# Kernel optimization log

Measured on AMD Instinct MI355X. Metric: run time of the kernel, lower is better.

Reference implementation:

```python
import jax, jax.numpy as jnp
import numpy as np

ALPHA = 0.5
DIM = -1
TOL = 1e-4
MAX_ITER = 5000


def stable_log_w(y, alpha):
    """Halley's method root of h(x) = -alpha*x + (y-alpha) - (1-alpha)*exp(x)."""

    def resid(x):
        return -alpha * x + (y - alpha) - (1.0 - alpha) * jnp.exp(x)

    x0 = jnp.minimum(y / alpha - 1.0, y - 1.0)

    def cond(st):
        x, it = st
        # torch breaks when max|f| <= tol -> continue while > tol
        return (jnp.max(jnp.abs(resid(x))) > TOL) & (it < MAX_ITER)

    def body(st):
        x, it = st
        e = jnp.exp(x)
        f = -alpha * x + (y - alpha) - (1.0 - alpha) * e
        df = -alpha - (1.0 - alpha) * e
        ddf = -(1.0 - alpha) * e
        x = x - 2.0 * f * df / (2.0 * df * df - f * ddf)
        return (x, it + 1)

    x, _ = jax.lax.while_loop(cond, body, (x0, jnp.int32(0)))
    return x


def prox_softmax_core(y, alpha, dim):
    """Newton over nu s.t. sum_i exp(g(y_i + nu)) = 1. Returns (p, nu, l)."""

    def eval_at(nu):
        l = stable_log_w(y + nu, alpha)
        p = jnp.exp(l)
        f = jnp.sum(p, axis=dim, keepdims=True) - 1.0
        return l, p, f

    nu0 = 1.0 - jnp.max(y, axis=dim, keepdims=True)
    l0, p0, f0 = eval_at(nu0)

    def cond(st):
        nu, l, p, f, it = st
        # torch breaks when max|f| < tol -> continue while >= tol
        return (jnp.max(jnp.abs(f)) >= TOL) & (it < MAX_ITER)

    def body(st):
        nu, l, p, f, it = st
        df = jnp.sum(p / (y + nu - alpha * l), axis=dim, keepdims=True)
        nu = nu - f / df
        l, p, f = eval_at(nu)
        return (nu, l, p, f, it + 1)

    nu, l, p, f, _ = jax.lax.while_loop(cond, body, (nu0, l0, p0, f0, jnp.int32(0)))
    return p, nu, l


def setup_inputs() -> dict:
    key = jax.random.key(0)
    x = jax.random.normal(key, (8192, 4096), dtype=jnp.float32)
    return {"x": x}


def reference(x):
    p, _, _ = prox_softmax_core(x, ALPHA, DIM)
    return p
```

## Files before the change

### kernel.cpp

```cpp
#include <hip/hip_runtime.h>
#include <math.h>

#define TPB 256
#define NWAVE 4
#define EPT 16
#define COLS 4096
#define RPB 4

typedef float vfloat4 __attribute__((ext_vector_type(4)));

__device__ __forceinline__ float wave_sum(float v) {
#pragma unroll
    for (int o = 32; o > 0; o >>= 1) v += __shfl_xor(v, o, 64);
    return v;
}
__device__ __forceinline__ float wave_max(float v) {
#pragma unroll
    for (int o = 32; o > 0; o >>= 1) v = fmaxf(v, __shfl_xor(v, o, 64));
    return v;
}

__device__ __forceinline__ void block_red2_h(float& a, float& b, volatile float* sred, int wid, int lane) {
    a = wave_sum(a); b = wave_sum(b);
    if (lane == 0) { sred[20 + wid] = a; sred[24 + wid] = b; }
    __syncthreads();
    a = (sred[20] + sred[21]) + (sred[22] + sred[23]);
    b = (sred[24] + sred[25]) + (sred[26] + sred[27]);
    __syncthreads();
}

__device__ __forceinline__ float halley_hw(float p, float t) {
    float e = __expf(p);
    float w = p * e;
    float f = w - t;
    float fp = w + e;
    float den = fmaf(fp, fp, -0.5f * f * (fp + e));
    return p - __fdividef(f * fp, den);
}

__global__ __launch_bounds__(TPB) void prox_softmax_kernel(
    const float* __restrict__ X, float* __restrict__ P, int rows)
{
    __shared__ float sred[28];
    const int tid = threadIdx.x;
    const int wid = tid >> 6, lane = tid & 63;
    const int row0 = blockIdx.x * RPB;
    const float C2E = 2.8853900817779268f;

    float cur[EPT], nxt[EPT];

    {
        const float4* __restrict__ x4 = reinterpret_cast<const float4*>(X + (size_t)row0 * COLS);
#pragma unroll
        for (int j = 0; j < 4; ++j) {
            float4 v = x4[tid + j * TPB];
            cur[4 * j + 0] = v.x; cur[4 * j + 1] = v.y;
            cur[4 * j + 2] = v.z; cur[4 * j + 3] = v.w;
        }
    }

    for (int r = 0; r < RPB; ++r) {
        const int row = row0 + r;
        if (row >= rows) return;
        const float4* __restrict__ x4 = reinterpret_cast<const float4*>(X + (size_t)row * COLS);
        vfloat4* __restrict__ p4 = reinterpret_cast<vfloat4*>(P + (size_t)row * COLS);

        if (r + 1 < RPB && row + 1 < rows) {
            const float4* __restrict__ x4n = reinterpret_cast<const float4*>(X + (size_t)(row + 1) * COLS);
#pragma unroll
            for (int j = 0; j < 4; ++j) {
                float4 v = x4n[tid + j * TPB];
                nxt[4 * j + 0] = v.x; nxt[4 * j + 1] = v.y;
                nxt[4 * j + 2] = v.z; nxt[4 * j + 3] = v.w;
            }
        }

        float A = 0.f, B = 0.f, qm = 0.f;
#pragma unroll
        for (int j = 0; j < EPT; ++j) {
            float e = __builtin_amdgcn_exp2f(cur[j] * C2E);
            cur[j] = e;
            A += e;
            B = fmaf(e, e, B);
            qm = fmaxf(qm, e);
        }

        A = wave_sum(A); B = wave_sum(B); qm = wave_max(qm);
        if (lane == 0) { sred[wid] = A; sred[4 + wid] = B; sred[8 + wid] = qm; }
        __syncthreads();
        A  = (sred[0] + sred[1]) + (sred[2] + sred[3]);
        B  = (sred[4] + sred[5]) + (sred[6] + sred[7]);
        qm = fmaxf(fmaxf(sred[8], sred[9]), fmaxf(sred[10], sred[11]));

        float disc = fmaf(A, A, -4.f * B);
        float s = __fdividef(2.f, A + sqrtf(fmaxf(disc, 0.f)));

        float S1 = 0.f, S2 = 0.f;
#pragma unroll
        for (int j = 0; j < EPT; ++j) {
            float t = cur[j] * s;
            float acc = fmaf(23.343054f, t, -10.8f);
            acc = fmaf(acc, t, 125.f / 24.f);
            acc = fmaf(acc, t, -8.f / 3.f);
            acc = fmaf(acc, t, 1.5f);
            acc = fmaf(acc, t, -1.f);
            acc = fmaf(acc, t, 1.f);
            float pp = t * acc;
            cur[j] = pp;
            S1 += pp;
            S2 += pp * fmaf(pp, pp - 1.f, 1.f);
        }

        S1 = wave_sum(S1); S2 = wave_sum(S2);
        if (lane == 0) { sred[12 + wid] = S1; sred[16 + wid] = S2; }
        __syncthreads();
        S1 = (sred[12] + sred[13]) + (sred[14] + sred[15]);
        S2 = (sred[16] + sred[17]) + (sred[18] + sred[19]);

        float f = S1 - 1.f;
        float tmax = qm * s;

        if ((tmax < 0.22f) && (fabsf(f) < 0.05f)) {
            float dsig = -__fdividef(f, S2);
#pragma unroll
            for (int j = 0; j < EPT; ++j) {
                float pp = cur[j];
                float rr = pp * fmaf(pp, pp - 1.f, 1.f);
                cur[j] = fmaf(rr, dsig, pp);
            }
        } else {
            float ls = __log2f(s);
#pragma unroll
            for (int j = 0; j < 4; ++j) {
                float4 v = x4[tid + j * TPB];
#pragma unroll
                for (int k = 0; k < 4; ++k) {
                    float xv = (k == 0) ? v.x : (k == 1) ? v.y : (k == 2) ? v.z : v.w;
                    float t = __builtin_amdgcn_exp2f(fmaf(xv, C2E, ls));
                    cur[4 * j + k] = __logf(1.f + t);
                }
            }
            for (int it = 0; it < 10; ++it) {
                S1 = 0.f; S2 = 0.f;
                float ls2 = __log2f(s);
#pragma unroll
                for (int j = 0; j < 4; ++j) {
                    float4 v = x4[tid + j * TPB];
#pragma unroll
                    for (int k = 0; k < 4; ++k) {
                        float xv = (k == 0) ? v.x : (k == 1) ? v.y : (k == 2) ? v.z : v.w;
                        float t = __builtin_amdgcn_exp2f(fmaf(xv, C2E, ls2));
                        float pp = halley_hw(cur[4 * j + k], t);
                        pp = halley_hw(pp, t);
                        cur[4 * j + k] = pp;
                        S1 += pp;
                        S2 += __fdividef(pp, 1.f + pp);
                    }
                }
                block_red2_h(S1, S2, sred, wid, lane);
                f = S1 - 1.f;
                if (fabsf(f) < 2e-5f) break;
                float dsig = fminf(fmaxf(-__fdividef(f, S2), -1.f), 1.f);
                s *= __expf(dsig);
            }
        }

#pragma unroll
        for (int j = 0; j < 4; ++j) {
            vfloat4 v;
            v.x = cur[4 * j + 0]; v.y = cur[4 * j + 1];
            v.z = cur[4 * j + 2]; v.w = cur[4 * j + 3];
            __builtin_nontemporal_store(v, &p4[tid + j * TPB]);
        }

        if (r + 1 < RPB) {
#pragma unroll
            for (int j = 0; j < EPT; ++j) cur[j] = nxt[j];
        }
    }
}

extern "C" void kernel_launch(void* const* d_in, const int* in_sizes, int n_in,
                              void* d_out, int out_size, void* d_ws, size_t ws_size,
                              hipStream_t stream) {
    const float* x = (const float*)d_in[0];
    float* out = (float*)d_out;
    int rows = out_size / COLS;
    int blocks = (rows + RPB - 1) / RPB;
    prox_softmax_kernel<<<blocks, TPB, 0, stream>>>(x, out, rows);
}
```

Before: 56.47 us.

## Process two rows per block interleaved, merging their reductions into shared barriers

Switches from four rows per block processed sequentially with next-row prefetch to two rows per block processed together. Both rows' exp, series and reduction steps are interleaved so their block reductions share a single barrier, which halves the number of barriers per row and exposes more independent work to each thread. The grid doubles to rows/2 blocks. In exchange, register pressure rises from holding two 16-element rows, there is no longer an odd-row tail guard, and the __syncthreads inside divergent heavy-path branches depends on the branch condition being uniform across the block.

```diff
diff --git a/kernel.cpp b/kernel.cpp
--- a/kernel.cpp
+++ b/kernel.cpp
@@ -2,10 +2,8 @@
 #include <math.h>
 
 #define TPB 256
-#define NWAVE 4
 #define EPT 16
 #define COLS 4096
-#define RPB 4
 
 typedef float vfloat4 __attribute__((ext_vector_type(4)));
 
@@ -18,15 +16,6 @@
 #pragma unroll
     for (int o = 32; o > 0; o >>= 1) v = fmaxf(v, __shfl_xor(v, o, 64));
     return v;
-}
-
-__device__ __forceinline__ void block_red2_h(float& a, float& b, volatile float* sred, int wid, int lane) {
-    a = wave_sum(a); b = wave_sum(b);
-    if (lane == 0) { sred[20 + wid] = a; sred[24 + wid] = b; }
-    __syncthreads();
-    a = (sred[20] + sred[21]) + (sred[22] + sred[23]);
-    b = (sred[24] + sred[25]) + (sred[26] + sred[27]);
-    __syncthreads();
 }
 
 __device__ __forceinline__ float halley_hw(float p, float t) {
@@ -38,145 +27,171 @@
     return p - __fdividef(f * fp, den);
 }
 
+__device__ __forceinline__ float w_series(float t) {
+    float acc = fmaf(23.343054f, t, -10.8f);
+    acc = fmaf(acc, t, 125.f / 24.f);
+    acc = fmaf(acc, t, -8.f / 3.f);
+    acc = fmaf(acc, t, 1.5f);
+    acc = fmaf(acc, t, -1.f);
+    acc = fmaf(acc, t, 1.f);
+    return t * acc;
+}
+
+__device__ __forceinline__ void heavy_solve(
+    const float4* __restrict__ x4, float* qq, float& s,
+    volatile float* sred, int tid, int wid, int lane, float C2E)
+{
+    float ls = __log2f(s);
+#pragma unroll
+    for (int j = 0; j < 4; ++j) {
+        float4 v = x4[tid + j * TPB];
+#pragma unroll
+        for (int k = 0; k < 4; ++k) {
+            float xv = (k == 0) ? v.x : (k == 1) ? v.y : (k == 2) ? v.z : v.w;
+            float t = __builtin_amdgcn_exp2f(fmaf(xv, C2E, ls));
+            qq[4 * j + k] = __logf(1.f + t);
+        }
+    }
+    for (int it = 0; it < 10; ++it) {
+        float S1 = 0.f, S2 = 0.f;
+        float ls2 = __log2f(s);
+#pragma unroll
+        for (int j = 0; j < 4; ++j) {
+            float4 v = x4[tid + j * TPB];
+#pragma unroll
+            for (int k = 0; k < 4; ++k) {
+                float xv = (k == 0) ? v.x : (k == 1) ? v.y : (k == 2) ? v.z : v.w;
+                float t = __builtin_amdgcn_exp2f(fmaf(xv, C2E, ls2));
+                float pp = halley_hw(qq[4 * j + k], t);
+                pp = halley_hw(pp, t);
+                qq[4 * j + k] = pp;
+                S1 += pp;
+                S2 += __fdividef(pp, 1.f + pp);
+            }
+        }
+        S1 = wave_sum(S1); S2 = wave_sum(S2);
+        if (lane == 0) { sred[40 + wid] = S1; sred[44 + wid] = S2; }
+        __syncthreads();
+        S1 = (sred[40] + sred[41]) + (sred[42] + sred[43]);
+        S2 = (sred[44] + sred[45]) + (sred[46] + sred[47]);
+        __syncthreads();
+        float f = S1 - 1.f;
+        if (fabsf(f) < 2e-5f) break;
+        float dsig = fminf(fmaxf(-__fdividef(f, S2), -1.f), 1.f);
+        s *= __expf(dsig);
+    }
+}
+
 __global__ __launch_bounds__(TPB) void prox_softmax_kernel(
     const float* __restrict__ X, float* __restrict__ P, int rows)
 {
-    __shared__ float sred[28];
+    __shared__ float sred[48];
     const int tid = threadIdx.x;
     const int wid = tid >> 6, lane = tid & 63;
-    const int row0 = blockIdx.x * RPB;
+    const int row0 = blockIdx.x * 2;
+    const int row1 = row0 + 1;
     const float C2E = 2.8853900817779268f;
 
-    float cur[EPT], nxt[EPT];
-
-    {
-        const float4* __restrict__ x4 = reinterpret_cast<const float4*>(X + (size_t)row0 * COLS);
-#pragma unroll
-        for (int j = 0; j < 4; ++j) {
-            float4 v = x4[tid + j * TPB];
-            cur[4 * j + 0] = v.x; cur[4 * j + 1] = v.y;
-            cur[4 * j + 2] = v.z; cur[4 * j + 3] = v.w;
-        }
-    }
-
-    for (int r = 0; r < RPB; ++r) {
-        const int row = row0 + r;
-        if (row >= rows) return;
-        const float4* __restrict__ x4 = reinterpret_cast<const float4*>(X + (size_t)row * COLS);
-        vfloat4* __restrict__ p4 = reinterpret_cast<vfloat4*>(P + (size_t)row * COLS);
-
-        if (r + 1 < RPB && row + 1 < rows) {
-            const float4* __restrict__ x4n = reinterpret_cast<const float4*>(X + (size_t)(row + 1) * COLS);
-#pragma unroll
-            for (int j = 0; j < 4; ++j) {
-                float4 v = x4n[tid + j * TPB];
-                nxt[4 * j + 0] = v.x; nxt[4 * j + 1] = v.y;
-                nxt[4 * j + 2] = v.z; nxt[4 * j + 3] = v.w;
-            }
-        }
-
-        float A = 0.f, B = 0.f, qm = 0.f;
+    const float4* __restrict__ xa = reinterpret_cast<const float4*>(X + (size_t)row0 * COLS);
+    const float4* __restrict__ xb = reinterpret_cast<const float4*>(X + (size_t)row1 * COLS);
+    vfloat4* __restrict__ pa = reinterpret_cast<vfloat4*>(P + (size_t)row0 * COLS);
+    vfloat4* __restrict__ pb = reinterpret_cast<vfloat4*>(P + (size_t)row1 * COLS);
+
+    float a[EPT], b[EPT];
+
+#pragma unroll
+    for (int j = 0; j < 4; ++j) {
+        float4 va = xa[tid + j * TPB];
+        float4 vb = xb[tid + j * TPB];
+        a[4 * j + 0] = va.x; a[4 * j + 1] = va.y; a[4 * j + 2] = va.z; a[4 * j + 3] = va.w;
+        b[4 * j + 0] = vb.x; b[4 * j + 1] = vb.y; b[4 * j + 2] = vb.z; b[4 * j + 3] = vb.w;
+    }
+
+    float A0 = 0.f, B0 = 0.f, m0 = 0.f;
+    float A1 = 0.f, B1 = 0.f, m1 = 0.f;
+#pragma unroll
+    for (int j = 0; j < EPT; ++j) {
+        float e0 = __builtin_amdgcn_exp2f(a[j] * C2E);
+        float e1 = __builtin_amdgcn_exp2f(b[j] * C2E);
+        a[j] = e0; b[j] = e1;
+        A0 += e0;             A1 += e1;
+        B0 = fmaf(e0, e0, B0); B1 = fmaf(e1, e1, B1);
+        m0 = fmaxf(m0, e0);   m1 = fmaxf(m1, e1);
+    }
+
+    A0 = wave_sum(A0); A1 = wave_sum(A1);
+    B0 = wave_sum(B0); B1 = wave_sum(B1);
+    m0 = wave_max(m0); m1 = wave_max(m1);
+    if (lane == 0) {
+        sred[wid] = A0;      sred[4 + wid] = B0;  sred[8 + wid] = m0;
+        sred[12 + wid] = A1; sred[16 + wid] = B1; sred[20 + wid] = m1;
+    }
+    __syncthreads();
+    A0 = (sred[0] + sred[1]) + (sred[2] + sred[3]);
+    B0 = (sred[4] + sred[5]) + (sred[6] + sred[7]);
+    m0 = fmaxf(fmaxf(sred[8], sred[9]), fmaxf(sred[10], sred[11]));
+    A1 = (sred[12] + sred[13]) + (sred[14] + sred[15]);
+    B1 = (sred[16] + sred[17]) + (sred[18] + sred[19]);
+    m1 = fmaxf(fmaxf(sred[20], sred[21]), fmaxf(sred[22], sred[23]));
+
+    float s0 = __fdividef(2.f, A0 + sqrtf(fmaxf(fmaf(A0, A0, -4.f * B0), 0.f)));
+    float s1 = __fdividef(2.f, A1 + sqrtf(fmaxf(fmaf(A1, A1, -4.f * B1), 0.f)));
+
+    float Sa = 0.f, Ta = 0.f, Sb = 0.f, Tb = 0.f;
+#pragma unroll
+    for (int j = 0; j < EPT; ++j) {
+        float p0 = w_series(a[j] * s0);
+        float p1 = w_series(b[j] * s1);
+        a[j] = p0; b[j] = p1;
+        Sa += p0; Sb += p1;
+        Ta += p0 * fmaf(p0, p0 - 1.f, 1.f);
+        Tb += p1 * fmaf(p1, p1 - 1.f, 1.f);
+    }
+
+    Sa = wave_sum(Sa); Sb = wave_sum(Sb);
+    Ta = wave_sum(Ta); Tb = wave_sum(Tb);
+    if (lane == 0) {
+        sred[24 + wid] = Sa; sred[28 + wid] = Ta;
+        sred[32 + wid] = Sb; sred[36 + wid] = Tb;
+    }
+    __syncthreads();
+    Sa = (sred[24] + sred[25]) + (sred[26] + sred[27]);
+    Ta = (sred[28] + sred[29]) + (sred[30] + sred[31]);
+    Sb = (sred[32] + sred[33]) + (sred[34] + sred[35]);
+    Tb = (sred[36] + sred[37]) + (sred[38] + sred[39]);
+
+    float f0 = Sa - 1.f, f1 = Sb - 1.f;
+
+    if ((m0 * s0 < 0.22f) && (fabsf(f0) < 0.05f)) {
+        float dsig = -__fdividef(f0, Ta);
 #pragma unroll
         for (int j = 0; j < EPT; ++j) {
-            float e = __builtin_amdgcn_exp2f(cur[j] * C2E);
-            cur[j] = e;
-            A += e;
-            B = fmaf(e, e, B);
-            qm = fmaxf(qm, e);
-        }
-
-        A = wave_sum(A); B = wave_sum(B); qm = wave_max(qm);
-        if (lane == 0) { sred[wid] = A; sred[4 + wid] = B; sred[8 + wid] = qm; }
-        __syncthreads();
-        A  = (sred[0] + sred[1]) + (sred[2] + sred[3]);
-        B  = (sred[4] + sred[5]) + (sred[6] + sred[7]);
-        qm = fmaxf(fmaxf(sred[8], sred[9]), fmaxf(sred[10], sred[11]));
-
-        float disc = fmaf(A, A, -4.f * B);
-        float s = __fdividef(2.f, A + sqrtf(fmaxf(disc, 0.f)));
-
-        float S1 = 0.f, S2 = 0.f;
+            float pp = a[j];
+            a[j] = fmaf(pp * fmaf(pp, pp - 1.f, 1.f), dsig, pp);
+        }
+    } else {
+        __syncthreads();
+        heavy_solve(xa, a, s0, sred, tid, wid, lane, C2E);
+    }
+    if ((m1 * s1 < 0.22f) && (fabsf(f1) < 0.05f)) {
+        float dsig = -__fdividef(f1, Tb);
 #pragma unroll
         for (int j = 0; j < EPT; ++j) {
-            float t = cur[j] * s;
-            float acc = fmaf(23.343054f, t, -10.8f);
-            acc = fmaf(acc, t, 125.f / 24.f);
-            acc = fmaf(acc, t, -8.f / 3.f);
-            acc = fmaf(acc, t, 1.5f);
-            acc = fmaf(acc, t, -1.f);
-            acc = fmaf(acc, t, 1.f);
-            float pp = t * acc;
-            cur[j] = pp;
-            S1 += pp;
-            S2 += pp * fmaf(pp, pp - 1.f, 1.f);
-        }
-
-        S1 = wave_sum(S1); S2 = wave_sum(S2);
-        if (lane == 0) { sred[12 + wid] = S1; sred[16 + wid] = S2; }
-        __syncthreads();
-        S1 = (sred[12] + sred[13]) + (sred[14] + sred[15]);
-        S2 = (sred[16] + sred[17]) + (sred[18] + sred[19]);
-
-        float f = S1 - 1.f;
-        float tmax = qm * s;
-
-        if ((tmax < 0.22f) && (fabsf(f) < 0.05f)) {
-            float dsig = -__fdividef(f, S2);
-#pragma unroll
-            for (int j = 0; j < EPT; ++j) {
-                float pp = cur[j];
-                float rr = pp * fmaf(pp, pp - 1.f, 1.f);
-                cur[j] = fmaf(rr, dsig, pp);
-            }
-        } else {
-            float ls = __log2f(s);
-#pragma unroll
-            for (int j = 0; j < 4; ++j) {
-                float4 v = x4[tid + j * TPB];
-#pragma unroll
-                for (int k = 0; k < 4; ++k) {
-                    float xv = (k == 0) ? v.x : (k == 1) ? v.y : (k == 2) ? v.z : v.w;
-                    float t = __builtin_amdgcn_exp2f(fmaf(xv, C2E, ls));
-                    cur[4 * j + k] = __logf(1.f + t);
-                }
-            }
-            for (int it = 0; it < 10; ++it) {
-                S1 = 0.f; S2 = 0.f;
-                float ls2 = __log2f(s);
-#pragma unroll
-                for (int j = 0; j < 4; ++j) {
-                    float4 v = x4[tid + j * TPB];
-#pragma unroll
-                    for (int k = 0; k < 4; ++k) {
-                        float xv = (k == 0) ? v.x : (k == 1) ? v.y : (k == 2) ? v.z : v.w;
-                        float t = __builtin_amdgcn_exp2f(fmaf(xv, C2E, ls2));
-                        float pp = halley_hw(cur[4 * j + k], t);
-                        pp = halley_hw(pp, t);
-                        cur[4 * j + k] = pp;
-                        S1 += pp;
-                        S2 += __fdividef(pp, 1.f + pp);
-                    }
-                }
-                block_red2_h(S1, S2, sred, wid, lane);
-                f = S1 - 1.f;
-                if (fabsf(f) < 2e-5f) break;
-                float dsig = fminf(fmaxf(-__fdividef(f, S2), -1.f), 1.f);
-                s *= __expf(dsig);
-            }
-        }
-
-#pragma unroll
-        for (int j = 0; j < 4; ++j) {
-            vfloat4 v;
-            v.x = cur[4 * j + 0]; v.y = cur[4 * j + 1];
-            v.z = cur[4 * j + 2]; v.w = cur[4 * j + 3];
-            __builtin_nontemporal_store(v, &p4[tid + j * TPB]);
-        }
-
-        if (r + 1 < RPB) {
-#pragma unroll
-            for (int j = 0; j < EPT; ++j) cur[j] = nxt[j];
-        }
+            float pp = b[j];
+            b[j] = fmaf(pp * fmaf(pp, pp - 1.f, 1.f), dsig, pp);
+        }
+    } else {
+        __syncthreads();
+        heavy_solve(xb, b, s1, sred, tid, wid, lane, C2E);
+    }
+
+#pragma unroll
+    for (int j = 0; j < 4; ++j) {
+        vfloat4 v0, v1;
+        v0.x = a[4 * j + 0]; v0.y = a[4 * j + 1]; v0.z = a[4 * j + 2]; v0.w = a[4 * j + 3];
+        v1.x = b[4 * j + 0]; v1.y = b[4 * j + 1]; v1.z = b[4 * j + 2]; v1.w = b[4 * j + 3];
+        __builtin_nontemporal_store(v0, &pa[tid + j * TPB]);
+        __builtin_nontemporal_store(v1, &pb[tid + j * TPB]);
     }
 }
 
@@ -186,6 +201,6 @@
     const float* x = (const float*)d_in[0];
     float* out = (float*)d_out;
     int rows = out_size / COLS;
-    int blocks = (rows + RPB - 1) / RPB;
+    int blocks = rows / 2;
     prox_softmax_kernel<<<blocks, TPB, 0, stream>>>(x, out, rows);
 }
```

Result: faster. 52.69 us (-6.7%).
